# Optimization experiments

Hardware: AMD Instinct MI355X
Metric: run time of the kernel (lower is better)

Reference implementation:

```python
import jax, jax.numpy as jnp
import numpy as np

EPS = 1e-5  # F.instance_norm default eps


def _inorm(x, axis):
    # instance norm (no affine), biased variance, over `axis`
    m = jnp.mean(x, axis=axis, keepdims=True)
    v = jnp.mean((x - m) ** 2, axis=axis, keepdims=True)
    return (x - m) * jax.lax.rsqrt(v + EPS)


def setup_inputs() -> dict:
    key = jax.random.key(0)
    ks = jax.random.split(key, 8)
    C, N, H, W = 256, 8192, 96, 96
    wscale = C ** -0.5  # keep logits in a sane range
    q = jax.random.normal(ks[0], (N, C), jnp.float32)
    k = jax.random.normal(ks[1], (1, C, H, W), jnp.float32)
    qw = jax.random.normal(ks[2], (C, C), jnp.float32) * wscale
    qb = jax.random.normal(ks[3], (C,), jnp.float32) * 0.1
    kw = jax.random.normal(ks[4], (C, C), jnp.float32) * wscale
    kb = jax.random.normal(ks[5], (C,), jnp.float32) * 0.1
    sw = jax.random.normal(ks[6], (C, C), jnp.float32) * wscale
    sb = jax.random.normal(ks[7], (C,), jnp.float32) * 0.1
    return {"q": q, "k": k, "qw": qw, "qb": qb, "kw": kw, "kb": kb, "sw": sw, "sb": sb}


def reference(q, k, qw, qb, kw, kb, sw, sb):
    # q: (N, C) content features; k: (1, C, H, W) style features
    C = q.shape[1]
    qc = q.T                       # (C, N)  == q.T.unsqueeze(0) without batch dim
    st = k[0].reshape(C, -1)       # (C, HW) style values (flattened)

    qn = _inorm(qc, 1)             # instance norm over N per channel
    qe = (qw @ qn + qb[:, None]).T # Conv1d 1x1 -> (N, C)

    kn = _inorm(st, 1)             # instance norm over H*W per channel
    ke = kw @ kn + kb[:, None]     # Conv2d 1x1 -> (C, HW)

    se = (sw @ st + sb[:, None]).T # Conv2d 1x1 -> (HW, C)

    scale = C ** -0.5
    attn = jax.nn.softmax((qe @ ke) * scale, axis=-1)   # (N, HW)

    mean = attn @ se                                    # (N, C)
    var = jax.nn.relu(attn @ (se * se) - mean * mean)   # (N, C)
    std = jnp.sqrt(var)

    cs = qn.T * std + mean          # instance_norm(c) * std + mean, (N, C)
    return cs
```

## Files before the change

### kernel.cpp

```cpp
#include <hip/hip_runtime.h>

typedef __attribute__((ext_vector_type(8))) short short8;
typedef __attribute__((ext_vector_type(4))) float float4v;

#define CDIM 256
#define NQ   8192
#define HWN  9216

static __device__ __forceinline__ unsigned short f2bf(float f) {
  union { float f; unsigned int i; } v; v.f = f;
  unsigned int r = v.i + 0x7FFFu + ((v.i >> 16) & 1u);
  return (unsigned short)(r >> 16);
}

__global__ __launch_bounds__(256) void stats_q1_kernel(const float* __restrict__ q,
                                                       float* __restrict__ pq, float* __restrict__ pq2) {
  int b = blockIdx.x, t = threadIdx.x;
  const float4* q4 = (const float4*)(q + (size_t)b * 32 * CDIM);
  float sx = 0, sy = 0, sz = 0, sw = 0, tx = 0, ty = 0, tz = 0, tw = 0;
  for (int i = t; i < 32 * 64; i += 256) {
    float4 v = q4[i];
    sx += v.x; sy += v.y; sz += v.z; sw += v.w;
    tx += v.x * v.x; ty += v.y * v.y; tz += v.z * v.z; tw += v.w * v.w;
  }
  __shared__ float4 sA[256], sB[256];
  sA[t] = make_float4(sx, sy, sz, sw); sB[t] = make_float4(tx, ty, tz, tw);
  __syncthreads();
  if (t < 64) {
    float4 a = sA[t], b2 = sB[t];
    #pragma unroll
    for (int r = 1; r < 4; r++) {
      float4 u = sA[t + r * 64], w2 = sB[t + r * 64];
      a.x += u.x; a.y += u.y; a.z += u.z; a.w += u.w;
      b2.x += w2.x; b2.y += w2.y; b2.z += w2.z; b2.w += w2.w;
    }
    ((float4*)pq)[b * 64 + t] = a;
    ((float4*)pq2)[b * 64 + t] = b2;
  }
}

__global__ __launch_bounds__(256) void stats_k_kernel(const float* __restrict__ k0,
                                                      float* __restrict__ mk, float* __restrict__ rk) {
  __shared__ float rs[256], rs2[256];
  int c = blockIdx.x, t = threadIdx.x;
  float s = 0.f, s2 = 0.f;
  const float4* row = (const float4*)(k0 + (size_t)c * HWN);
  for (int j = t; j < HWN / 4; j += 256) {
    float4 v = row[j];
    s += v.x + v.y + v.z + v.w;
    s2 += v.x * v.x + v.y * v.y + v.z * v.z + v.w * v.w;
  }
  rs[t] = s; rs2[t] = s2; __syncthreads();
  for (int off = 128; off > 0; off >>= 1) {
    if (t < off) { rs[t] += rs[t + off]; rs2[t] += rs2[t + off]; }
    __syncthreads();
  }
  if (t == 0) {
    float mean = rs[0] / (float)HWN;
    float var = rs2[0] / (float)HWN - mean * mean;
    mk[c] = mean; rk[c] = rsqrtf(fmaxf(var, 0.f) + 1e-5f);
  }
}

__global__ __launch_bounds__(256) void cvt3q2_kernel(const float* __restrict__ qw, const float* __restrict__ kw,
                                                     const float* __restrict__ sw,
                                                     unsigned short* __restrict__ qwb, unsigned short* __restrict__ kwb,
                                                     unsigned short* __restrict__ swb,
                                                     const float* __restrict__ pq, const float* __restrict__ pq2,
                                                     float* __restrict__ mq, float* __restrict__ rq) {
  int b = blockIdx.x;
  if (b < 192) {
    int which = b >> 6;
    const float* src = which == 0 ? qw : (which == 1 ? kw : sw);
    unsigned short* dst = which == 0 ? qwb : (which == 1 ? kwb : swb);
    int i = (b & 63) * 256 + threadIdx.x;
    float4 v = ((const float4*)src)[i];
    union { unsigned short o[4]; uint2 u; } w;
    w.o[0] = f2bf(v.x); w.o[1] = f2bf(v.y); w.o[2] = f2bf(v.z); w.o[3] = f2bf(v.w);
    ((uint2*)dst)[i] = w.u;
  } else {
    int c = threadIdx.x;
    float s = 0, s2 = 0;
    for (int bb = 0; bb < 256; bb++) { s += pq[bb * 256 + c]; s2 += pq2[bb * 256 + c]; }
    float mean = s / (float)NQ;
    float var = s2 / (float)NQ - mean * mean;
    mq[c] = mean; rq[c] = rsqrtf(fmaxf(var, 0.f) + 1e-5f);
  }
}

__global__ __launch_bounds__(256) void ktrans_kernel(const float* __restrict__ k0,
                                                     const float* __restrict__ mk, const float* __restrict__ rk,
                                                     unsigned short* __restrict__ stT, unsigned short* __restrict__ stn) {
  __shared__ float tile[32][33];
  int p0 = blockIdx.x * 32, c0 = blockIdx.y * 32;
  int t = threadIdx.x;
  int pl = t & 31, cl = t >> 5;
  #pragma unroll
  for (int r = 0; r < 4; r++) {
    int c = cl + r * 8;
    tile[c][pl] = k0[(size_t)(c0 + c) * HWN + p0 + pl];
  }
  __syncthreads();
  int cl2 = t & 31, pl2 = t >> 5;
  float mean = mk[c0 + cl2], rinv = rk[c0 + cl2];
  #pragma unroll
  for (int r = 0; r < 4; r++) {
    int p = pl2 + r * 8;
    float f = tile[cl2][p];
    stT[(size_t)(p0 + p) * CDIM + c0 + cl2] = f2bf(f);
    stn[(size_t)(p0 + p) * CDIM + c0 + cl2] = f2bf((f - mean) * rinv);
  }
}

__global__ __launch_bounds__(256) void gemm_q_kernel(const float* __restrict__ qf,
                                                     const float* __restrict__ mq, const float* __restrict__ rq,
                                                     const unsigned short* __restrict__ Bp,
                                                     const float* __restrict__ bias,
                                                     unsigned short* __restrict__ out0) {
  int t = threadIdx.x;
  int w = t >> 6, lane = t & 63, g = lane >> 4, li = lane & 15;
  int m0 = blockIdx.x * 64;
  float4v acc[16];
  #pragma unroll
  for (int i = 0; i < 16; i++) acc[i] = (float4v){0.f, 0.f, 0.f, 0.f};
  const float* abase = qf + (size_t)(m0 + w * 16 + li) * CDIM + g * 8;
  #pragma unroll
  for (int kc = 0; kc < 8; kc++) {
    int c0 = kc * 32 + g * 8;
    float4 f0 = *(const float4*)(abase + kc * 32);
    float4 f1 = *(const float4*)(abase + kc * 32 + 4);
    float4 m0v = *(const float4*)(mq + c0), m1v = *(const float4*)(mq + c0 + 4);
    float4 r0v = *(const float4*)(rq + c0), r1v = *(const float4*)(rq + c0 + 4);
    union { unsigned short o[8]; short8 s; } a;
    a.o[0] = f2bf((f0.x - m0v.x) * r0v.x); a.o[1] = f2bf((f0.y - m0v.y) * r0v.y);
    a.o[2] = f2bf((f0.z - m0v.z) * r0v.z); a.o[3] = f2bf((f0.w - m0v.w) * r0v.w);
    a.o[4] = f2bf((f1.x - m1v.x) * r1v.x); a.o[5] = f2bf((f1.y - m1v.y) * r1v.y);
    a.o[6] = f2bf((f1.z - m1v.z) * r1v.z); a.o[7] = f2bf((f1.w - m1v.w) * r1v.w);
    #pragma unroll
    for (int ct = 0; ct < 16; ct++) {
      short8 b = *(const short8*)(Bp + (size_t)(ct * 16 + li) * CDIM + kc * 32 + g * 8);
      acc[ct] = __builtin_amdgcn_mfma_f32_16x16x32_bf16(a.s, b, acc[ct], 0, 0, 0);
    }
  }
  #pragma unroll
  for (int ct = 0; ct < 16; ct++) {
    int col = ct * 16 + li;
    #pragma unroll
    for (int j = 0; j < 4; j++) {
      int row = m0 + w * 16 + g * 4 + j;
      float v = (acc[ct][j] + bias[col]) * (0.0625f * 1.4426950408889634f);
      out0[(size_t)row * CDIM + col] = f2bf(v);
    }
  }
}

template<int MODE>
__global__ __launch_bounds__(256) void gemm_kernel(const unsigned short* __restrict__ Ap,
                                                   const unsigned short* __restrict__ Bp,
                                                   const float* __restrict__ bias,
                                                   unsigned short* __restrict__ out0,
                                                   unsigned short* __restrict__ out1) {
  int t = threadIdx.x;
  int w = t >> 6, lane = t & 63, g = lane >> 4, li = lane & 15;
  int m0 = blockIdx.x * 64, n0 = blockIdx.y * 256;
  float4v acc[16];
  #pragma unroll
  for (int i = 0; i < 16; i++) acc[i] = (float4v){0.f, 0.f, 0.f, 0.f};
  const unsigned short* abase = Ap + (size_t)(m0 + w * 16 + li) * CDIM + g * 8;
  #pragma unroll
  for (int kc = 0; kc < 8; kc++) {
    short8 a = *(const short8*)(abase + kc * 32);
    #pragma unroll
    for (int ct = 0; ct < 16; ct++) {
      short8 b = *(const short8*)(Bp + (size_t)(n0 + ct * 16 + li) * CDIM + kc * 32 + g * 8);
      acc[ct] = __builtin_amdgcn_mfma_f32_16x16x32_bf16(a, b, acc[ct], 0, 0, 0);
    }
  }
  #pragma unroll
  for (int ct = 0; ct < 16; ct++) {
    int col = n0 + ct * 16 + li;
    #pragma unroll
    for (int j = 0; j < 4; j++) {
      int row = m0 + w * 16 + g * 4 + j;
      float v = acc[ct][j];
      if (MODE == 1) {
        v += bias[col];
        out0[(size_t)row * CDIM + col] = f2bf(v);
      } else {
        v += bias[row];
        out0[(size_t)row * HWN + col] = f2bf(v);
        out1[(size_t)row * HWN + col] = f2bf(v * v);
      }
    }
  }
}

static __device__ __forceinline__ void issue_K(int p0, int w, int lane,
                                               const unsigned short* __restrict__ Km,
                                               unsigned short* K_buf) {
  #pragma unroll
  for (int j2 = 0; j2 < 2; j2++) {
    int i16 = (j2 * 8 + w) * 64 + lane;
    int row = i16 >> 5;
    int chc = (i16 & 31) ^ (row & 15);
    const unsigned short* src = Km + (size_t)(p0 + row) * CDIM + chc * 8;
    unsigned short* dst = K_buf + (j2 * 8 + w) * 512;
    __builtin_amdgcn_global_load_lds((const __attribute__((address_space(1))) unsigned int*)src,
                                     (__attribute__((address_space(3))) unsigned int*)dst, 16, 0, 0);
  }
}

static __device__ __forceinline__ void issue_V(int p0, int w, int lane,
                                               const unsigned short* __restrict__ VseT,
                                               const unsigned short* __restrict__ Vse2T,
                                               unsigned short* V_buf) {
  #pragma unroll
  for (int j2 = 0; j2 < 4; j2++) {
    int i16 = (j2 * 8 + w) * 64 + lane;
    int vrow = i16 >> 2;
    int chunk = (i16 & 3) ^ ((vrow >> 1) & 3);
    const unsigned short* src = (vrow < 256 ? VseT + (size_t)vrow * HWN
                                            : Vse2T + (size_t)(vrow - 256) * HWN) + p0 + chunk * 8;
    unsigned short* dst = V_buf + (j2 * 8 + w) * 512;
    __builtin_amdgcn_global_load_lds((const __attribute__((address_space(1))) unsigned int*)src,
                                     (__attribute__((address_space(3))) unsigned int*)dst, 16, 0, 0);
  }
}

__global__ __launch_bounds__(512, 1) void attn_kernel(const unsigned short* __restrict__ Qs,
                                                      const unsigned short* __restrict__ Km,
                                                      const unsigned short* __restrict__ VseT,
                                                      const unsigned short* __restrict__ Vse2T,
                                                      float* __restrict__ Op, float2* __restrict__ ml,
                                                      int tiles_per_g, int G) {
  __shared__ __align__(16) unsigned short K_lds[2][32 * 256];
  __shared__ __align__(16) unsigned short V_lds[3][512 * 32];
  __shared__ __align__(16) unsigned short P_lds[2][128 * 40];
  __shared__ float corr_lds[128];
  __shared__ int needflag[8];

  const int t = threadIdx.x;
  const int w = t >> 6, lane = t & 63;
  const int g4 = lane >> 4, li = lane & 15;

  int bid = blockIdx.x, qb, g;
  if (G == 4) { g = (bid & 7) >> 1; qb = ((bid & 1) << 5) + (bid >> 3); }
  else        { g = bid % G;        qb = bid / G; }
  const int n0 = qb * 128;
  const int p_begin = g * tiles_per_g * 32;

  short8 qf[8];
  {
    const unsigned short* qbase = Qs + (size_t)(n0 + w * 16 + li) * CDIM + g4 * 8;
    #pragma unroll
    for (int kc = 0; kc < 8; kc++) qf[kc] = *(const short8*)(qbase + kc * 32);
  }
  float4v O[8][4];
  #pragma unroll
  for (int r = 0; r < 8; r++)
    #pragma unroll
    for (int v = 0; v < 4; v++) O[r][v] = (float4v){0.f, 0.f, 0.f, 0.f};
  float4v s_acc = (float4v){0.f, 0.f, 0.f, 0.f};
  float m[4] = {-1e30f, -1e30f, -1e30f, -1e30f};
  const short8 ones = (short8){0x3F80, 0x3F80, 0x3F80, 0x3F80, 0x3F80, 0x3F80, 0x3F80, 0x3F80};

#define PV_BLOCK(P_buf, V_buf)                                                               \
  {                                                                                          \
    short8 vb[4];                                                                            \
    _Pragma("unroll")                                                                        \
    for (int v = 0; v < 4; v++) {                                                            \
      int vrow = w * 64 + v * 16 + li;                                                       \
      vb[v] = *(const short8*)((const char*)(V_buf) + vrow * 64 + ((g4 ^ ((vrow >> 1) & 3)) << 4)); \
    }                                                                                        \
    __builtin_amdgcn_s_setprio(1);                                                           \
    _Pragma("unroll")                                                                        \
    for (int r = 0; r < 8; r++) {                                                            \
      short8 pa = *(const short8*)((P_buf) + (r * 16 + li) * 40 + g4 * 8);                   \
      if (r == w) s_acc = __builtin_amdgcn_mfma_f32_16x16x32_bf16(pa, ones, s_acc, 0, 0, 0); \
      _Pragma("unroll")                                                                      \
      for (int v = 0; v < 4; v++)                                                            \
        O[r][v] = __builtin_amdgcn_mfma_f32_16x16x32_bf16(pa, vb[v], O[r][v], 0, 0, 0);      \
    }                                                                                        \
    __builtin_amdgcn_s_setprio(0);                                                           \
  }

  issue_K(p_begin, w, lane, Km, K_lds[0]);
  issue_V(p_begin, w, lane, VseT, Vse2T, V_lds[0]);

  for (int it = 0; it < tiles_per_g; ++it) {
    if (it + 1 < tiles_per_g) {
      issue_K(p_begin + (it + 1) * 32, w, lane, Km, K_lds[(it + 1) & 1]);
      issue_V(p_begin + (it + 1) * 32, w, lane, VseT, Vse2T, V_lds[(it + 1) % 3]);
      asm volatile("s_waitcnt vmcnt(6)" ::: "memory");
    } else {
      asm volatile("s_waitcnt vmcnt(0)" ::: "memory");
    }
    __builtin_amdgcn_s_barrier();
    asm volatile("" ::: "memory");

    const unsigned short* Kc = K_lds[it & 1];
    float4v S0 = (float4v){0.f, 0.f, 0.f, 0.f}, S1 = (float4v){0.f, 0.f, 0.f, 0.f};
    __builtin_amdgcn_s_setprio(1);
    #pragma unroll
    for (int kc = 0; kc < 8; kc++) {
      int c = kc * 4 + g4;
      short8 b0 = *(const short8*)((const char*)Kc + li * 512 + ((c ^ li) << 4));
      short8 b1 = *(const short8*)((const char*)Kc + (16 + li) * 512 + ((c ^ li) << 4));
      S0 = __builtin_amdgcn_mfma_f32_16x16x32_bf16(qf[kc], b0, S0, 0, 0, 0);
      S1 = __builtin_amdgcn_mfma_f32_16x16x32_bf16(qf[kc], b1, S1, 0, 0, 0);
    }
    __builtin_amdgcn_s_setprio(0);

    if (it > 0) PV_BLOCK(P_lds[(it - 1) & 1], V_lds[(it - 1) % 3]);

    float pmax[4], corr[4];
    #pragma unroll
    for (int j = 0; j < 4; j++) {
      float mx = fmaxf(S0[j], S1[j]);
      #pragma unroll
      for (int msk = 1; msk < 16; msk <<= 1) mx = fmaxf(mx, __shfl_xor(mx, msk, 64));
      pmax[j] = mx;
    }
    int needs = ((pmax[0] > m[0] + 8.f) || (pmax[1] > m[1] + 8.f) ||
                 (pmax[2] > m[2] + 8.f) || (pmax[3] > m[3] + 8.f)) ? 1 : 0;
    if (needs) {
      #pragma unroll
      for (int j = 0; j < 4; j++) {
        float mn = fmaxf(m[j], pmax[j]);
        corr[j] = exp2f(m[j] - mn);
        m[j] = mn;
      }
    } else {
      corr[0] = corr[1] = corr[2] = corr[3] = 1.f;
    }
    int wany = __any(needs) ? 1 : 0;
    unsigned short* Pw = P_lds[it & 1];
    #pragma unroll
    for (int j = 0; j < 4; j++) {
      float e0 = exp2f(S0[j] - m[j]);
      float e1 = exp2f(S1[j] - m[j]);
      int row = w * 16 + g4 * 4 + j;
      Pw[row * 40 + li] = f2bf(e0);
      Pw[row * 40 + 16 + li] = f2bf(e1);
      if (li == 0) corr_lds[row] = corr[j];
    }
    if (lane == 0) needflag[w] = wany;

    asm volatile("s_waitcnt lgkmcnt(0)" ::: "memory");
    __builtin_amdgcn_s_barrier();
    asm volatile("" ::: "memory");

    int any = __any(needflag[lane & 7] != 0);
    if (any) {
      #pragma unroll
      for (int j = 0; j < 4; j++) s_acc[j] *= corr[j];
      #pragma unroll
      for (int r = 0; r < 8; r++) {
        float c0 = corr_lds[r * 16 + g4 * 4 + 0];
        float c1 = corr_lds[r * 16 + g4 * 4 + 1];
        float c2 = corr_lds[r * 16 + g4 * 4 + 2];
        float c3 = corr_lds[r * 16 + g4 * 4 + 3];
        #pragma unroll
        for (int v = 0; v < 4; v++) {
          O[r][v][0] *= c0; O[r][v][1] *= c1; O[r][v][2] *= c2; O[r][v][3] *= c3;
        }
      }
    }
  }

  {
    int tl = tiles_per_g - 1;
    PV_BLOCK(P_lds[tl & 1], V_lds[tl % 3]);
  }
#undef PV_BLOCK

  #pragma unroll
  for (int r = 0; r < 8; r++) {
    #pragma unroll
    for (int v = 0; v < 4; v++) {
      #pragma unroll
      for (int j = 0; j < 4; j++) {
        int n = n0 + r * 16 + g4 * 4 + j;
        int vd = w * 64 + v * 16 + li;
        Op[((size_t)g * NQ + n) * 512 + vd] = O[r][v][j];
      }
    }
  }
  if (li == 0) {
    #pragma unroll
    for (int j = 0; j < 4; j++) {
      int n = n0 + w * 16 + g4 * 4 + j;
      ml[(size_t)g * NQ + n] = make_float2(m[j], s_acc[j]);
    }
  }
}

__global__ __launch_bounds__(256) void combine_kernel(const float* __restrict__ Op, const float2* __restrict__ ml,
                                                      const float* __restrict__ q,
                                                      const float* __restrict__ mq, const float* __restrict__ rq,
                                                      float* __restrict__ out, int G) {
  int n = blockIdx.x, t = threadIdx.x;
  __shared__ float w_s[8];
  if (t == 0) {
    float mstar = -1e30f;
    float mg[8], lg[8];
    for (int g = 0; g < G; g++) {
      float2 v = ml[(size_t)g * NQ + n];
      mg[g] = v.x; lg[g] = v.y;
      mstar = fmaxf(mstar, v.x);
    }
    float L = 0.f;
    for (int g = 0; g < G; g++) L += lg[g] * exp2f(mg[g] - mstar);
    float Li = 1.f / L;
    for (int g = 0; g < G; g++) w_s[g] = exp2f(mg[g] - mstar) * Li;
  }
  __syncthreads();
  int c = t;
  float of = 0.f, o2 = 0.f;
  for (int g = 0; g < G; g++) {
    size_t base = ((size_t)g * NQ + n) * 512;
    float wg = w_s[g];
    of += wg * Op[base + c];
    o2 += wg * Op[base + 256 + c];
  }
  float mean = of;
  float var = fmaxf(o2 - mean * mean, 0.f);
  float sd = sqrtf(var);
  float qn = (q[(size_t)n * CDIM + c] - mq[c]) * rq[c];
  out[(size_t)n * CDIM + c] = qn * sd + mean;
}

extern "C" void kernel_launch(void* const* d_in, const int* in_sizes, int n_in,
                              void* d_out, int out_size, void* d_ws, size_t ws_size,
                              hipStream_t stream) {
  const float* q  = (const float*)d_in[0];
  const float* k0 = (const float*)d_in[1];
  const float* qw = (const float*)d_in[2];
  const float* qb = (const float*)d_in[3];
  const float* kw = (const float*)d_in[4];
  const float* kb = (const float*)d_in[5];
  const float* sw = (const float*)d_in[6];
  const float* sb = (const float*)d_in[7];
  float* out = (float*)d_out;

  char* ws = (char*)d_ws;
  float* mq = (float*)ws;  ws += 1024;
  float* rq = (float*)ws;  ws += 1024;
  float* mk = (float*)ws;  ws += 1024;
  float* rk = (float*)ws;  ws += 1024;
  float* pq  = (float*)ws; ws += 256 * 256 * 4;
  float* pq2 = (float*)ws; ws += 256 * 256 * 4;
  unsigned short* qwb = (unsigned short*)ws; ws += 65536 * 2;
  unsigned short* kwb = (unsigned short*)ws; ws += 65536 * 2;
  unsigned short* swb = (unsigned short*)ws; ws += 65536 * 2;
  unsigned short* Qs   = (unsigned short*)ws; ws += (size_t)NQ * CDIM * 2;
  unsigned short* stT  = (unsigned short*)ws; ws += (size_t)HWN * CDIM * 2;
  unsigned short* stn  = (unsigned short*)ws; ws += (size_t)HWN * CDIM * 2;
  unsigned short* Km   = (unsigned short*)ws; ws += (size_t)HWN * CDIM * 2;
  unsigned short* VseT = (unsigned short*)ws; ws += (size_t)HWN * CDIM * 2;
  unsigned short* Vse2T = stn;

  size_t base_used = (size_t)(ws - (char*)d_ws);
  int G = 4;
  const int gcand[3] = {4, 2, 1};
  for (int i = 0; i < 3; i++) {
    G = gcand[i];
    size_t need = base_used + (size_t)G * ((size_t)NQ * 512 * 4 + (size_t)NQ * 8);
    if (need <= ws_size) break;
  }
  float*  Opart = (float*)ws;                 ws += (size_t)G * NQ * 512 * 4;
  float2* mlp   = (float2*)ws;                ws += (size_t)G * NQ * 8;
  int tiles_per_g = (HWN / 32) / G;

  stats_q1_kernel<<<256, 256, 0, stream>>>(q, pq, pq2);
  stats_k_kernel<<<256, 256, 0, stream>>>(k0, mk, rk);
  cvt3q2_kernel<<<193, 256, 0, stream>>>(qw, kw, sw, qwb, kwb, swb, pq, pq2, mq, rq);
  ktrans_kernel<<<dim3(HWN / 32, CDIM / 32), 256, 0, stream>>>(k0, mk, rk, stT, stn);
  gemm_q_kernel<<<dim3(NQ / 64), 256, 0, stream>>>(q, mq, rq, qwb, qb, Qs);
  gemm_kernel<1><<<dim3(HWN / 64, 1), 256, 0, stream>>>(stn, kwb, kb, Km, nullptr);
  gemm_kernel<2><<<dim3(CDIM / 64, HWN / 256), 256, 0, stream>>>(swb, stT, sb, VseT, Vse2T);
  attn_kernel<<<dim3(64 * G), 512, 0, stream>>>(Qs, Km, VseT, Vse2T, Opart, mlp, tiles_per_g, G);
  combine_kernel<<<NQ, 256, 0, stream>>>(Opart, mlp, q, mq, rq, out, G);
}
```

Measured before the change: 342.6 us.

## Fuse prep kernels, fold style stats into weights, restructure attention PV per-wave

```diff
diff --git a/kernel.cpp b/kernel.cpp
--- a/kernel.cpp
+++ b/kernel.cpp
@@ -13,84 +13,99 @@
   return (unsigned short)(r >> 16);
 }
 
-__global__ __launch_bounds__(256) void stats_q1_kernel(const float* __restrict__ q,
-                                                       float* __restrict__ pq, float* __restrict__ pq2) {
+__global__ __launch_bounds__(256) void stats_all_kernel(const float* __restrict__ q, const float* __restrict__ k0,
+                                                        float* __restrict__ pq, float* __restrict__ pq2,
+                                                        float* __restrict__ mk, float* __restrict__ rk,
+                                                        float* __restrict__ sdk) {
   int b = blockIdx.x, t = threadIdx.x;
-  const float4* q4 = (const float4*)(q + (size_t)b * 32 * CDIM);
-  float sx = 0, sy = 0, sz = 0, sw = 0, tx = 0, ty = 0, tz = 0, tw = 0;
-  for (int i = t; i < 32 * 64; i += 256) {
-    float4 v = q4[i];
-    sx += v.x; sy += v.y; sz += v.z; sw += v.w;
-    tx += v.x * v.x; ty += v.y * v.y; tz += v.z * v.z; tw += v.w * v.w;
-  }
-  __shared__ float4 sA[256], sB[256];
-  sA[t] = make_float4(sx, sy, sz, sw); sB[t] = make_float4(tx, ty, tz, tw);
-  __syncthreads();
-  if (t < 64) {
-    float4 a = sA[t], b2 = sB[t];
-    #pragma unroll
-    for (int r = 1; r < 4; r++) {
-      float4 u = sA[t + r * 64], w2 = sB[t + r * 64];
-      a.x += u.x; a.y += u.y; a.z += u.z; a.w += u.w;
-      b2.x += w2.x; b2.y += w2.y; b2.z += w2.z; b2.w += w2.w;
-    }
-    ((float4*)pq)[b * 64 + t] = a;
-    ((float4*)pq2)[b * 64 + t] = b2;
-  }
-}
-
-__global__ __launch_bounds__(256) void stats_k_kernel(const float* __restrict__ k0,
-                                                      float* __restrict__ mk, float* __restrict__ rk) {
-  __shared__ float rs[256], rs2[256];
-  int c = blockIdx.x, t = threadIdx.x;
-  float s = 0.f, s2 = 0.f;
-  const float4* row = (const float4*)(k0 + (size_t)c * HWN);
-  for (int j = t; j < HWN / 4; j += 256) {
-    float4 v = row[j];
-    s += v.x + v.y + v.z + v.w;
-    s2 += v.x * v.x + v.y * v.y + v.z * v.z + v.w * v.w;
-  }
-  rs[t] = s; rs2[t] = s2; __syncthreads();
-  for (int off = 128; off > 0; off >>= 1) {
-    if (t < off) { rs[t] += rs[t + off]; rs2[t] += rs2[t + off]; }
+  if (b < 256) {
+    const float4* q4 = (const float4*)(q + (size_t)b * 32 * CDIM);
+    float sx = 0, sy = 0, sz = 0, sw = 0, tx = 0, ty = 0, tz = 0, tw = 0;
+    for (int i = t; i < 32 * 64; i += 256) {
+      float4 v = q4[i];
+      sx += v.x; sy += v.y; sz += v.z; sw += v.w;
+      tx += v.x * v.x; ty += v.y * v.y; tz += v.z * v.z; tw += v.w * v.w;
+    }
+    __shared__ float4 sA[256], sB[256];
+    sA[t] = make_float4(sx, sy, sz, sw); sB[t] = make_float4(tx, ty, tz, tw);
     __syncthreads();
-  }
-  if (t == 0) {
-    float mean = rs[0] / (float)HWN;
-    float var = rs2[0] / (float)HWN - mean * mean;
-    mk[c] = mean; rk[c] = rsqrtf(fmaxf(var, 0.f) + 1e-5f);
-  }
-}
-
-__global__ __launch_bounds__(256) void cvt3q2_kernel(const float* __restrict__ qw, const float* __restrict__ kw,
-                                                     const float* __restrict__ sw,
+    if (t < 64) {
+      float4 a = sA[t], b2 = sB[t];
+      #pragma unroll
+      for (int r = 1; r < 4; r++) {
+        float4 u = sA[t + r * 64], w2 = sB[t + r * 64];
+        a.x += u.x; a.y += u.y; a.z += u.z; a.w += u.w;
+        b2.x += w2.x; b2.y += w2.y; b2.z += w2.z; b2.w += w2.w;
+      }
+      ((float4*)pq)[b * 64 + t] = a;
+      ((float4*)pq2)[b * 64 + t] = b2;
+    }
+  } else {
+    __shared__ float rs[256], rs2[256];
+    int c = b - 256;
+    float s = 0.f, s2 = 0.f;
+    const float4* row = (const float4*)(k0 + (size_t)c * HWN);
+    for (int j = t; j < HWN / 4; j += 256) {
+      float4 v = row[j];
+      s += v.x + v.y + v.z + v.w;
+      s2 += v.x * v.x + v.y * v.y + v.z * v.z + v.w * v.w;
+    }
+    rs[t] = s; rs2[t] = s2; __syncthreads();
+    for (int off = 128; off > 0; off >>= 1) {
+      if (t < off) { rs[t] += rs[t + off]; rs2[t] += rs2[t + off]; }
+      __syncthreads();
+    }
+    if (t == 0) {
+      float mean = rs[0] / (float)HWN;
+      float var = fmaxf(rs2[0] / (float)HWN - mean * mean, 0.f);
+      mk[c] = mean; rk[c] = rsqrtf(var + 1e-5f); sdk[c] = sqrtf(var + 1e-5f);
+    }
+  }
+}
+
+__global__ __launch_bounds__(256) void cvtall_kernel(const float* __restrict__ qw, const float* __restrict__ kw,
+                                                     const float* __restrict__ sw, const float* __restrict__ sb,
                                                      unsigned short* __restrict__ qwb, unsigned short* __restrict__ kwb,
-                                                     unsigned short* __restrict__ swb,
+                                                     unsigned short* __restrict__ swb2,
+                                                     const float* __restrict__ sdk, const float* __restrict__ mk,
                                                      const float* __restrict__ pq, const float* __restrict__ pq2,
-                                                     float* __restrict__ mq, float* __restrict__ rq) {
-  int b = blockIdx.x;
-  if (b < 192) {
-    int which = b >> 6;
-    const float* src = which == 0 ? qw : (which == 1 ? kw : sw);
-    unsigned short* dst = which == 0 ? qwb : (which == 1 ? kwb : swb);
-    int i = (b & 63) * 256 + threadIdx.x;
+                                                     float* __restrict__ mq, float* __restrict__ rq,
+                                                     float* __restrict__ bias2) {
+  int b = blockIdx.x, t = threadIdx.x;
+  if (b < 128) {
+    const float* src = b < 64 ? qw : kw;
+    unsigned short* dst = b < 64 ? qwb : kwb;
+    int i = (b & 63) * 256 + t;
     float4 v = ((const float4*)src)[i];
     union { unsigned short o[4]; uint2 u; } w;
     w.o[0] = f2bf(v.x); w.o[1] = f2bf(v.y); w.o[2] = f2bf(v.z); w.o[3] = f2bf(v.w);
     ((uint2*)dst)[i] = w.u;
-  } else {
-    int c = threadIdx.x;
+  } else if (b < 192) {
+    int i = (b - 128) * 256 + t;
+    int c0 = (i * 4) & 255;
+    float4 v = ((const float4*)sw)[i];
+    union { unsigned short o[4]; uint2 u; } w;
+    w.o[0] = f2bf(v.x * sdk[c0 + 0]); w.o[1] = f2bf(v.y * sdk[c0 + 1]);
+    w.o[2] = f2bf(v.z * sdk[c0 + 2]); w.o[3] = f2bf(v.w * sdk[c0 + 3]);
+    ((uint2*)swb2)[i] = w.u;
+  } else if (b == 192) {
+    int c = t;
     float s = 0, s2 = 0;
     for (int bb = 0; bb < 256; bb++) { s += pq[bb * 256 + c]; s2 += pq2[bb * 256 + c]; }
     float mean = s / (float)NQ;
     float var = s2 / (float)NQ - mean * mean;
     mq[c] = mean; rq[c] = rsqrtf(fmaxf(var, 0.f) + 1e-5f);
+  } else {
+    int r = t;
+    float acc = 0.f;
+    for (int k = 0; k < 256; k++) acc += sw[r * 256 + k] * mk[k];
+    bias2[r] = acc + sb[r];
   }
 }
 
 __global__ __launch_bounds__(256) void ktrans_kernel(const float* __restrict__ k0,
                                                      const float* __restrict__ mk, const float* __restrict__ rk,
-                                                     unsigned short* __restrict__ stT, unsigned short* __restrict__ stn) {
+                                                     unsigned short* __restrict__ stn) {
   __shared__ float tile[32][33];
   int p0 = blockIdx.x * 32, c0 = blockIdx.y * 32;
   int t = threadIdx.x;
@@ -107,89 +122,99 @@
   for (int r = 0; r < 4; r++) {
     int p = pl2 + r * 8;
     float f = tile[cl2][p];
-    stT[(size_t)(p0 + p) * CDIM + c0 + cl2] = f2bf(f);
     stn[(size_t)(p0 + p) * CDIM + c0 + cl2] = f2bf((f - mean) * rinv);
   }
 }
 
-__global__ __launch_bounds__(256) void gemm_q_kernel(const float* __restrict__ qf,
-                                                     const float* __restrict__ mq, const float* __restrict__ rq,
-                                                     const unsigned short* __restrict__ Bp,
-                                                     const float* __restrict__ bias,
-                                                     unsigned short* __restrict__ out0) {
-  int t = threadIdx.x;
+__global__ __launch_bounds__(256) void gemms_kernel(const float* __restrict__ qf,
+                                                    const float* __restrict__ mq, const float* __restrict__ rq,
+                                                    const unsigned short* __restrict__ qwb, const float* __restrict__ qb,
+                                                    unsigned short* __restrict__ Qs,
+                                                    const unsigned short* __restrict__ stn,
+                                                    const unsigned short* __restrict__ kwb, const float* __restrict__ kb,
+                                                    unsigned short* __restrict__ Km,
+                                                    const unsigned short* __restrict__ swb2, const float* __restrict__ bias2,
+                                                    unsigned short* __restrict__ VseT, unsigned short* __restrict__ Vse2T) {
+  int b = blockIdx.x, t = threadIdx.x;
   int w = t >> 6, lane = t & 63, g = lane >> 4, li = lane & 15;
-  int m0 = blockIdx.x * 64;
   float4v acc[16];
   #pragma unroll
   for (int i = 0; i < 16; i++) acc[i] = (float4v){0.f, 0.f, 0.f, 0.f};
-  const float* abase = qf + (size_t)(m0 + w * 16 + li) * CDIM + g * 8;
-  #pragma unroll
-  for (int kc = 0; kc < 8; kc++) {
-    int c0 = kc * 32 + g * 8;
-    float4 f0 = *(const float4*)(abase + kc * 32);
-    float4 f1 = *(const float4*)(abase + kc * 32 + 4);
-    float4 m0v = *(const float4*)(mq + c0), m1v = *(const float4*)(mq + c0 + 4);
-    float4 r0v = *(const float4*)(rq + c0), r1v = *(const float4*)(rq + c0 + 4);
-    union { unsigned short o[8]; short8 s; } a;
-    a.o[0] = f2bf((f0.x - m0v.x) * r0v.x); a.o[1] = f2bf((f0.y - m0v.y) * r0v.y);
-    a.o[2] = f2bf((f0.z - m0v.z) * r0v.z); a.o[3] = f2bf((f0.w - m0v.w) * r0v.w);
-    a.o[4] = f2bf((f1.x - m1v.x) * r1v.x); a.o[5] = f2bf((f1.y - m1v.y) * r1v.y);
-    a.o[6] = f2bf((f1.z - m1v.z) * r1v.z); a.o[7] = f2bf((f1.w - m1v.w) * r1v.w);
+
+  if (b < 128) {
+    int m0 = b * 64;
+    const float* abase = qf + (size_t)(m0 + w * 16 + li) * CDIM + g * 8;
+    #pragma unroll
+    for (int kc = 0; kc < 8; kc++) {
+      int c0 = kc * 32 + g * 8;
+      float4 f0 = *(const float4*)(abase + kc * 32);
+      float4 f1 = *(const float4*)(abase + kc * 32 + 4);
+      float4 m0v = *(const float4*)(mq + c0), m1v = *(const float4*)(mq + c0 + 4);
+      float4 r0v = *(const float4*)(rq + c0), r1v = *(const float4*)(rq + c0 + 4);
+      union { unsigned short o[8]; short8 s; } a;
+      a.o[0] = f2bf((f0.x - m0v.x) * r0v.x); a.o[1] = f2bf((f0.y - m0v.y) * r0v.y);
+      a.o[2] = f2bf((f0.z - m0v.z) * r0v.z); a.o[3] = f2bf((f0.w - m0v.w) * r0v.w);
+      a.o[4] = f2bf((f1.x - m1v.x) * r1v.x); a.o[5] = f2bf((f1.y - m1v.y) * r1v.y);
+      a.o[6] = f2bf((f1.z - m1v.z) * r1v.z); a.o[7] = f2bf((f1.w - m1v.w) * r1v.w);
+      #pragma unroll
+      for (int ct = 0; ct < 16; ct++) {
+        short8 bb = *(const short8*)(qwb + (size_t)(ct * 16 + li) * CDIM + kc * 32 + g * 8);
+        acc[ct] = __builtin_amdgcn_mfma_f32_16x16x32_bf16(a.s, bb, acc[ct], 0, 0, 0);
+      }
+    }
     #pragma unroll
     for (int ct = 0; ct < 16; ct++) {
-      short8 b = *(const short8*)(Bp + (size_t)(ct * 16 + li) * CDIM + kc * 32 + g * 8);
-      acc[ct] = __builtin_amdgcn_mfma_f32_16x16x32_bf16(a.s, b, acc[ct], 0, 0, 0);
-    }
-  }
-  #pragma unroll
-  for (int ct = 0; ct < 16; ct++) {
-    int col = ct * 16 + li;
-    #pragma unroll
-    for (int j = 0; j < 4; j++) {
-      int row = m0 + w * 16 + g * 4 + j;
-      float v = (acc[ct][j] + bias[col]) * (0.0625f * 1.4426950408889634f);
-      out0[(size_t)row * CDIM + col] = f2bf(v);
-    }
-  }
-}
-
-template<int MODE>
-__global__ __launch_bounds__(256) void gemm_kernel(const unsigned short* __restrict__ Ap,
-                                                   const unsigned short* __restrict__ Bp,
-                                                   const float* __restrict__ bias,
-                                                   unsigned short* __restrict__ out0,
-                                                   unsigned short* __restrict__ out1) {
-  int t = threadIdx.x;
-  int w = t >> 6, lane = t & 63, g = lane >> 4, li = lane & 15;
-  int m0 = blockIdx.x * 64, n0 = blockIdx.y * 256;
-  float4v acc[16];
-  #pragma unroll
-  for (int i = 0; i < 16; i++) acc[i] = (float4v){0.f, 0.f, 0.f, 0.f};
-  const unsigned short* abase = Ap + (size_t)(m0 + w * 16 + li) * CDIM + g * 8;
-  #pragma unroll
-  for (int kc = 0; kc < 8; kc++) {
-    short8 a = *(const short8*)(abase + kc * 32);
+      int col = ct * 16 + li;
+      #pragma unroll
+      for (int j = 0; j < 4; j++) {
+        int row = m0 + w * 16 + g * 4 + j;
+        float v = (acc[ct][j] + qb[col]) * (0.0625f * 1.4426950408889634f);
+        Qs[(size_t)row * CDIM + col] = f2bf(v);
+      }
+    }
+  } else if (b < 272) {
+    int m0 = (b - 128) * 64;
+    const unsigned short* abase = stn + (size_t)(m0 + w * 16 + li) * CDIM + g * 8;
+    #pragma unroll
+    for (int kc = 0; kc < 8; kc++) {
+      short8 a = *(const short8*)(abase + kc * 32);
+      #pragma unroll
+      for (int ct = 0; ct < 16; ct++) {
+        short8 bb = *(const short8*)(kwb + (size_t)(ct * 16 + li) * CDIM + kc * 32 + g * 8);
+        acc[ct] = __builtin_amdgcn_mfma_f32_16x16x32_bf16(a, bb, acc[ct], 0, 0, 0);
+      }
+    }
     #pragma unroll
     for (int ct = 0; ct < 16; ct++) {
-      short8 b = *(const short8*)(Bp + (size_t)(n0 + ct * 16 + li) * CDIM + kc * 32 + g * 8);
-      acc[ct] = __builtin_amdgcn_mfma_f32_16x16x32_bf16(a, b, acc[ct], 0, 0, 0);
-    }
-  }
-  #pragma unroll
-  for (int ct = 0; ct < 16; ct++) {
-    int col = n0 + ct * 16 + li;
-    #pragma unroll
-    for (int j = 0; j < 4; j++) {
-      int row = m0 + w * 16 + g * 4 + j;
-      float v = acc[ct][j];
-      if (MODE == 1) {
-        v += bias[col];
-        out0[(size_t)row * CDIM + col] = f2bf(v);
-      } else {
-        v += bias[row];
-        out0[(size_t)row * HWN + col] = f2bf(v);
-        out1[(size_t)row * HWN + col] = f2bf(v * v);
+      int col = ct * 16 + li;
+      #pragma unroll
+      for (int j = 0; j < 4; j++) {
+        int row = m0 + w * 16 + g * 4 + j;
+        Km[(size_t)row * CDIM + col] = f2bf(acc[ct][j] + kb[col]);
+      }
+    }
+  } else {
+    int bb2 = b - 272;
+    int m0 = (bb2 & 3) * 64, n0 = (bb2 >> 2) * 256;
+    const unsigned short* abase = swb2 + (size_t)(m0 + w * 16 + li) * CDIM + g * 8;
+    #pragma unroll
+    for (int kc = 0; kc < 8; kc++) {
+      short8 a = *(const short8*)(abase + kc * 32);
+      #pragma unroll
+      for (int ct = 0; ct < 16; ct++) {
+        short8 bb = *(const short8*)(stn + (size_t)(n0 + ct * 16 + li) * CDIM + kc * 32 + g * 8);
+        acc[ct] = __builtin_amdgcn_mfma_f32_16x16x32_bf16(a, bb, acc[ct], 0, 0, 0);
+      }
+    }
+    #pragma unroll
+    for (int ct = 0; ct < 16; ct++) {
+      int col = n0 + ct * 16 + li;
+      #pragma unroll
+      for (int j = 0; j < 4; j++) {
+        int row = m0 + w * 16 + g * 4 + j;
+        float v = acc[ct][j] + bias2[row];
+        VseT[(size_t)row * HWN + col] = f2bf(v);
+        Vse2T[(size_t)row * HWN + col] = f2bf(v * v);
       }
     }
   }
@@ -217,10 +242,10 @@
   #pragma unroll
   for (int j2 = 0; j2 < 4; j2++) {
     int i16 = (j2 * 8 + w) * 64 + lane;
-    int vrow = i16 >> 2;
-    int chunk = (i16 & 3) ^ ((vrow >> 1) & 3);
-    const unsigned short* src = (vrow < 256 ? VseT + (size_t)vrow * HWN
-                                            : Vse2T + (size_t)(vrow - 256) * HWN) + p0 + chunk * 8;
+    int vd = i16 >> 2;
+    int gc = (i16 & 3) ^ ((vd ^ (vd >> 2)) & 3);
+    const unsigned short* src = (vd < 256 ? VseT + (size_t)vd * HWN
+                                          : Vse2T + (size_t)(vd - 256) * HWN) + p0 + gc * 8;
     unsigned short* dst = V_buf + (j2 * 8 + w) * 512;
     __builtin_amdgcn_global_load_lds((const __attribute__((address_space(1))) unsigned int*)src,
                                      (__attribute__((address_space(3))) unsigned int*)dst, 16, 0, 0);
@@ -234,10 +259,8 @@
                                                       float* __restrict__ Op, float2* __restrict__ ml,
                                                       int tiles_per_g, int G) {
   __shared__ __align__(16) unsigned short K_lds[2][32 * 256];
-  __shared__ __align__(16) unsigned short V_lds[3][512 * 32];
-  __shared__ __align__(16) unsigned short P_lds[2][128 * 40];
-  __shared__ float corr_lds[128];
-  __shared__ int needflag[8];
+  __shared__ __align__(16) unsigned short V_lds[2][512 * 32];
+  __shared__ __align__(16) unsigned short P_scr[8 * 640];
 
   const int t = threadIdx.x;
   const int w = t >> 6, lane = t & 63;
@@ -255,48 +278,24 @@
     #pragma unroll
     for (int kc = 0; kc < 8; kc++) qf[kc] = *(const short8*)(qbase + kc * 32);
   }
-  float4v O[8][4];
-  #pragma unroll
-  for (int r = 0; r < 8; r++)
-    #pragma unroll
-    for (int v = 0; v < 4; v++) O[r][v] = (float4v){0.f, 0.f, 0.f, 0.f};
+  float4v O[32];
+  #pragma unroll
+  for (int i = 0; i < 32; i++) O[i] = (float4v){0.f, 0.f, 0.f, 0.f};
   float4v s_acc = (float4v){0.f, 0.f, 0.f, 0.f};
   float m[4] = {-1e30f, -1e30f, -1e30f, -1e30f};
   const short8 ones = (short8){0x3F80, 0x3F80, 0x3F80, 0x3F80, 0x3F80, 0x3F80, 0x3F80, 0x3F80};
 
-#define PV_BLOCK(P_buf, V_buf)                                                               \
-  {                                                                                          \
-    short8 vb[4];                                                                            \
-    _Pragma("unroll")                                                                        \
-    for (int v = 0; v < 4; v++) {                                                            \
-      int vrow = w * 64 + v * 16 + li;                                                       \
-      vb[v] = *(const short8*)((const char*)(V_buf) + vrow * 64 + ((g4 ^ ((vrow >> 1) & 3)) << 4)); \
-    }                                                                                        \
-    __builtin_amdgcn_s_setprio(1);                                                           \
-    _Pragma("unroll")                                                                        \
-    for (int r = 0; r < 8; r++) {                                                            \
-      short8 pa = *(const short8*)((P_buf) + (r * 16 + li) * 40 + g4 * 8);                   \
-      if (r == w) s_acc = __builtin_amdgcn_mfma_f32_16x16x32_bf16(pa, ones, s_acc, 0, 0, 0); \
-      _Pragma("unroll")                                                                      \
-      for (int v = 0; v < 4; v++)                                                            \
-        O[r][v] = __builtin_amdgcn_mfma_f32_16x16x32_bf16(pa, vb[v], O[r][v], 0, 0, 0);      \
-    }                                                                                        \
-    __builtin_amdgcn_s_setprio(0);                                                           \
-  }
-
   issue_K(p_begin, w, lane, Km, K_lds[0]);
   issue_V(p_begin, w, lane, VseT, Vse2T, V_lds[0]);
 
   for (int it = 0; it < tiles_per_g; ++it) {
+    asm volatile("s_waitcnt vmcnt(0)" ::: "memory");
+    __builtin_amdgcn_s_barrier();
+    asm volatile("" ::: "memory");
     if (it + 1 < tiles_per_g) {
       issue_K(p_begin + (it + 1) * 32, w, lane, Km, K_lds[(it + 1) & 1]);
-      issue_V(p_begin + (it + 1) * 32, w, lane, VseT, Vse2T, V_lds[(it + 1) % 3]);
-      asm volatile("s_waitcnt vmcnt(6)" ::: "memory");
-    } else {
-      asm volatile("s_waitcnt vmcnt(0)" ::: "memory");
-    }
-    __builtin_amdgcn_s_barrier();
-    asm volatile("" ::: "memory");
+      issue_V(p_begin + (it + 1) * 32, w, lane, VseT, Vse2T, V_lds[(it + 1) & 1]);
+    }
 
     const unsigned short* Kc = K_lds[it & 1];
     float4v S0 = (float4v){0.f, 0.f, 0.f, 0.f}, S1 = (float4v){0.f, 0.f, 0.f, 0.f};
@@ -311,8 +310,6 @@
     }
     __builtin_amdgcn_s_setprio(0);
 
-    if (it > 0) PV_BLOCK(P_lds[(it - 1) & 1], V_lds[(it - 1) % 3]);
-
     float pmax[4], corr[4];
     #pragma unroll
     for (int j = 0; j < 4; j++) {
@@ -321,8 +318,8 @@
       for (int msk = 1; msk < 16; msk <<= 1) mx = fmaxf(mx, __shfl_xor(mx, msk, 64));
       pmax[j] = mx;
     }
-    int needs = ((pmax[0] > m[0] + 8.f) || (pmax[1] > m[1] + 8.f) ||
-                 (pmax[2] > m[2] + 8.f) || (pmax[3] > m[3] + 8.f)) ? 1 : 0;
+    int needs = ((pmax[0] > m[0] + 5.f) || (pmax[1] > m[1] + 5.f) ||
+                 (pmax[2] > m[2] + 5.f) || (pmax[3] > m[3] + 5.f)) ? 1 : 0;
     if (needs) {
       #pragma unroll
       for (int j = 0; j < 4; j++) {
@@ -330,60 +327,46 @@
         corr[j] = exp2f(m[j] - mn);
         m[j] = mn;
       }
-    } else {
-      corr[0] = corr[1] = corr[2] = corr[3] = 1.f;
-    }
-    int wany = __any(needs) ? 1 : 0;
-    unsigned short* Pw = P_lds[it & 1];
+    }
+    unsigned short* Pw = P_scr + w * 640;
     #pragma unroll
     for (int j = 0; j < 4; j++) {
       float e0 = exp2f(S0[j] - m[j]);
       float e1 = exp2f(S1[j] - m[j]);
-      int row = w * 16 + g4 * 4 + j;
+      int row = g4 * 4 + j;
       Pw[row * 40 + li] = f2bf(e0);
       Pw[row * 40 + 16 + li] = f2bf(e1);
-      if (li == 0) corr_lds[row] = corr[j];
-    }
-    if (lane == 0) needflag[w] = wany;
-
-    asm volatile("s_waitcnt lgkmcnt(0)" ::: "memory");
-    __builtin_amdgcn_s_barrier();
-    asm volatile("" ::: "memory");
-
-    int any = __any(needflag[lane & 7] != 0);
-    if (any) {
+    }
+    if (__any(needs)) {
       #pragma unroll
       for (int j = 0; j < 4; j++) s_acc[j] *= corr[j];
       #pragma unroll
-      for (int r = 0; r < 8; r++) {
-        float c0 = corr_lds[r * 16 + g4 * 4 + 0];
-        float c1 = corr_lds[r * 16 + g4 * 4 + 1];
-        float c2 = corr_lds[r * 16 + g4 * 4 + 2];
-        float c3 = corr_lds[r * 16 + g4 * 4 + 3];
-        #pragma unroll
-        for (int v = 0; v < 4; v++) {
-          O[r][v][0] *= c0; O[r][v][1] *= c1; O[r][v][2] *= c2; O[r][v][3] *= c3;
-        }
-      }
-    }
-  }
-
-  {
-    int tl = tiles_per_g - 1;
-    PV_BLOCK(P_lds[tl & 1], V_lds[tl % 3]);
-  }
-#undef PV_BLOCK
-
-  #pragma unroll
-  for (int r = 0; r < 8; r++) {
-    #pragma unroll
-    for (int v = 0; v < 4; v++) {
-      #pragma unroll
-      for (int j = 0; j < 4; j++) {
-        int n = n0 + r * 16 + g4 * 4 + j;
-        int vd = w * 64 + v * 16 + li;
-        Op[((size_t)g * NQ + n) * 512 + vd] = O[r][v][j];
-      }
+      for (int i = 0; i < 32; i++) {
+        O[i][0] *= corr[0]; O[i][1] *= corr[1]; O[i][2] *= corr[2]; O[i][3] *= corr[3];
+      }
+    }
+
+    short8 pa = *(const short8*)(Pw + li * 40 + g4 * 8);
+    const unsigned short* Vc = V_lds[it & 1];
+    __builtin_amdgcn_s_setprio(1);
+    s_acc = __builtin_amdgcn_mfma_f32_16x16x32_bf16(pa, ones, s_acc, 0, 0, 0);
+    #pragma unroll
+    for (int vt = 0; vt < 32; vt++) {
+      int vd = vt * 16 + li;
+      int kc2 = g4 ^ ((vd ^ (vd >> 2)) & 3);
+      short8 vb = *(const short8*)((const char*)Vc + vd * 64 + (kc2 << 4));
+      O[vt] = __builtin_amdgcn_mfma_f32_16x16x32_bf16(pa, vb, O[vt], 0, 0, 0);
+    }
+    __builtin_amdgcn_s_setprio(0);
+  }
+
+  #pragma unroll
+  for (int vt = 0; vt < 32; vt++) {
+    #pragma unroll
+    for (int j = 0; j < 4; j++) {
+      int n = n0 + w * 16 + g4 * 4 + j;
+      int vd = vt * 16 + li;
+      Op[((size_t)g * NQ + n) * 512 + vd] = O[vt][j];
     }
   }
   if (li == 0) {
@@ -399,9 +382,11 @@
                                                       const float* __restrict__ q,
                                                       const float* __restrict__ mq, const float* __restrict__ rq,
                                                       float* __restrict__ out, int G) {
-  int n = blockIdx.x, t = threadIdx.x;
-  __shared__ float w_s[8];
-  if (t == 0) {
+  int t = threadIdx.x;
+  int rl = t >> 6, j = t & 63;
+  int n = blockIdx.x * 4 + rl, c0 = j * 4;
+  __shared__ float wsm[4][8];
+  if (j == 0) {
     float mstar = -1e30f;
     float mg[8], lg[8];
     for (int g = 0; g < G; g++) {
@@ -412,22 +397,27 @@
     float L = 0.f;
     for (int g = 0; g < G; g++) L += lg[g] * exp2f(mg[g] - mstar);
     float Li = 1.f / L;
-    for (int g = 0; g < G; g++) w_s[g] = exp2f(mg[g] - mstar) * Li;
+    for (int g = 0; g < G; g++) wsm[rl][g] = exp2f(mg[g] - mstar) * Li;
   }
   __syncthreads();
-  int c = t;
-  float of = 0.f, o2 = 0.f;
+  float4 of = make_float4(0, 0, 0, 0), o2 = make_float4(0, 0, 0, 0);
   for (int g = 0; g < G; g++) {
     size_t base = ((size_t)g * NQ + n) * 512;
-    float wg = w_s[g];
-    of += wg * Op[base + c];
-    o2 += wg * Op[base + 256 + c];
-  }
-  float mean = of;
-  float var = fmaxf(o2 - mean * mean, 0.f);
-  float sd = sqrtf(var);
-  float qn = (q[(size_t)n * CDIM + c] - mq[c]) * rq[c];
-  out[(size_t)n * CDIM + c] = qn * sd + mean;
+    float wg = wsm[rl][g];
+    float4 a = *(const float4*)(Op + base + c0);
+    float4 b = *(const float4*)(Op + base + 256 + c0);
+    of.x += wg * a.x; of.y += wg * a.y; of.z += wg * a.z; of.w += wg * a.w;
+    o2.x += wg * b.x; o2.y += wg * b.y; o2.z += wg * b.z; o2.w += wg * b.w;
+  }
+  float4 qv = *(const float4*)(q + (size_t)n * CDIM + c0);
+  float4 mv = *(const float4*)(mq + c0);
+  float4 rv = *(const float4*)(rq + c0);
+  float4 ov;
+  ov.x = (qv.x - mv.x) * rv.x * sqrtf(fmaxf(o2.x - of.x * of.x, 0.f)) + of.x;
+  ov.y = (qv.y - mv.y) * rv.y * sqrtf(fmaxf(o2.y - of.y * of.y, 0.f)) + of.y;
+  ov.z = (qv.z - mv.z) * rv.z * sqrtf(fmaxf(o2.z - of.z * of.z, 0.f)) + of.z;
+  ov.w = (qv.w - mv.w) * rv.w * sqrtf(fmaxf(o2.w - of.w * of.w, 0.f)) + of.w;
+  *(float4*)(out + (size_t)n * CDIM + c0) = ov;
 }
 
 extern "C" void kernel_launch(void* const* d_in, const int* in_sizes, int n_in,
@@ -444,21 +434,22 @@
   float* out = (float*)d_out;
 
   char* ws = (char*)d_ws;
-  float* mq = (float*)ws;  ws += 1024;
-  float* rq = (float*)ws;  ws += 1024;
-  float* mk = (float*)ws;  ws += 1024;
-  float* rk = (float*)ws;  ws += 1024;
-  float* pq  = (float*)ws; ws += 256 * 256 * 4;
-  float* pq2 = (float*)ws; ws += 256 * 256 * 4;
-  unsigned short* qwb = (unsigned short*)ws; ws += 65536 * 2;
-  unsigned short* kwb = (unsigned short*)ws; ws += 65536 * 2;
-  unsigned short* swb = (unsigned short*)ws; ws += 65536 * 2;
-  unsigned short* Qs   = (unsigned short*)ws; ws += (size_t)NQ * CDIM * 2;
-  unsigned short* stT  = (unsigned short*)ws; ws += (size_t)HWN * CDIM * 2;
-  unsigned short* stn  = (unsigned short*)ws; ws += (size_t)HWN * CDIM * 2;
-  unsigned short* Km   = (unsigned short*)ws; ws += (size_t)HWN * CDIM * 2;
-  unsigned short* VseT = (unsigned short*)ws; ws += (size_t)HWN * CDIM * 2;
-  unsigned short* Vse2T = stn;
+  float* mq   = (float*)ws; ws += 1024;
+  float* rq   = (float*)ws; ws += 1024;
+  float* mk   = (float*)ws; ws += 1024;
+  float* rk   = (float*)ws; ws += 1024;
+  float* sdk  = (float*)ws; ws += 1024;
+  float* bias2= (float*)ws; ws += 1024;
+  float* pq   = (float*)ws; ws += 256 * 256 * 4;
+  float* pq2  = (float*)ws; ws += 256 * 256 * 4;
+  unsigned short* qwb  = (unsigned short*)ws; ws += 65536 * 2;
+  unsigned short* kwb  = (unsigned short*)ws; ws += 65536 * 2;
+  unsigned short* swb2 = (unsigned short*)ws; ws += 65536 * 2;
+  unsigned short* Qs    = (unsigned short*)ws; ws += (size_t)NQ * CDIM * 2;
+  unsigned short* stn   = (unsigned short*)ws; ws += (size_t)HWN * CDIM * 2;
+  unsigned short* Km    = (unsigned short*)ws; ws += (size_t)HWN * CDIM * 2;
+  unsigned short* VseT  = (unsigned short*)ws; ws += (size_t)HWN * CDIM * 2;
+  unsigned short* Vse2T = (unsigned short*)ws; ws += (size_t)HWN * CDIM * 2;
 
   size_t base_used = (size_t)(ws - (char*)d_ws);
   int G = 4;
@@ -472,13 +463,10 @@
   float2* mlp   = (float2*)ws;                ws += (size_t)G * NQ * 8;
   int tiles_per_g = (HWN / 32) / G;
 
-  stats_q1_kernel<<<256, 256, 0, stream>>>(q, pq, pq2);
-  stats_k_kernel<<<256, 256, 0, stream>>>(k0, mk, rk);
-  cvt3q2_kernel<<<193, 256, 0, stream>>>(qw, kw, sw, qwb, kwb, swb, pq, pq2, mq, rq);
-  ktrans_kernel<<<dim3(HWN / 32, CDIM / 32), 256, 0, stream>>>(k0, mk, rk, stT, stn);
-  gemm_q_kernel<<<dim3(NQ / 64), 256, 0, stream>>>(q, mq, rq, qwb, qb, Qs);
-  gemm_kernel<1><<<dim3(HWN / 64, 1), 256, 0, stream>>>(stn, kwb, kb, Km, nullptr);
-  gemm_kernel<2><<<dim3(CDIM / 64, HWN / 256), 256, 0, stream>>>(swb, stT, sb, VseT, Vse2T);
+  stats_all_kernel<<<512, 256, 0, stream>>>(q, k0, pq, pq2, mk, rk, sdk);
+  cvtall_kernel<<<194, 256, 0, stream>>>(qw, kw, sw, sb, qwb, kwb, swb2, sdk, mk, pq, pq2, mq, rq, bias2);
+  ktrans_kernel<<<dim3(HWN / 32, CDIM / 32), 256, 0, stream>>>(k0, mk, rk, stn);
+  gemms_kernel<<<416, 256, 0, stream>>>(q, mq, rq, qwb, qb, Qs, stn, kwb, kb, Km, swb2, bias2, VseT, Vse2T);
   attn_kernel<<<dim3(64 * G), 512, 0, stream>>>(Qs, Km, VseT, Vse2T, Opart, mlp, tiles_per_g, G);
-  combine_kernel<<<NQ, 256, 0, stream>>>(Opart, mlp, q, mq, rq, out, G);
-}
+  combine_kernel<<<NQ / 4, 256, 0, stream>>>(Opart, mlp, q, mq, rq, out, G);
+}
```

Result: faster. 304.4 us, median of 2 (-11.2%).
